# Kernel optimization log

Hardware: AMD Instinct MI355X
Metric: run time of the kernel (lower is better)

The kernel has to match this reference:

```python
import jax, jax.numpy as jnp
import numpy as np

B = 2048        # patients (segments)
K = 4           # images per patient
C = 1280        # backbone_out (tf_efficientnet_b0)
PAIRS = K * (K - 1) // 2  # torch.combinations -> 6
NCLS = 1
N_DROP = 5


def setup_inputs() -> dict:
    key = jax.random.key(0)
    ks = jax.random.split(key, 8)
    x = jax.random.normal(ks[0], (B * K, C), jnp.float32)  # detached backbone features
    ids2 = jnp.repeat(jnp.arange(B, dtype=jnp.int32), PAIRS)  # segment id per pair
    Wc = jax.random.normal(ks[1], (C, C, 2), jnp.float32) * 0.02  # Conv1d(C,C,k=2) weight
    bc = jnp.zeros((C,), jnp.float32)
    W0 = jax.random.normal(ks[2], (NCLS, C), jnp.float32) * 0.02
    b0 = jnp.zeros((NCLS,), jnp.float32)
    W1 = jax.random.normal(ks[3], (1, C), jnp.float32) * 0.02
    b1 = jnp.zeros((1,), jnp.float32)
    W2 = jax.random.normal(ks[4], (1, C), jnp.float32) * 0.02
    b2 = jnp.zeros((1,), jnp.float32)
    return dict(x=x, ids2=ids2, Wc=Wc, bc=bc, W0=W0, b0=b0, W1=W1, b1=b1, W2=W2, b2=b2)


def reference(x, ids2, Wc, bc, W0, b0, W1, b1, W2, b2):
    # --- pair combinations within each patient group of K images ---
    ii, jj = np.triu_indices(K, 1)               # static [PAIRS]
    xg = x.reshape(B, K, C)
    xa = xg[:, ii].reshape(B * PAIRS, C)         # first element of each pair
    xb = xg[:, jj].reshape(B * PAIRS, C)         # second element
    # Conv1d(C, C, kernel=2) over the length-2 pair sequence + ReLU
    xc = jax.nn.relu(xa @ Wc[:, :, 0].T + xb @ Wc[:, :, 1].T + bc)  # [P, C]

    # --- 5 fixed dropout masks (p=0.5, train-mode scaling) ---
    masks = jax.random.bernoulli(jax.random.key(42), 0.5,
                                 (N_DROP, xc.shape[0], C)).astype(xc.dtype) * 2.0
    xd = xc[None] * masks                        # [D, P, C]

    cnt = jax.ops.segment_sum(jnp.ones_like(ids2, dtype=xc.dtype),
                              ids2, num_segments=B)  # [B], == PAIRS

    def agg(W, b):
        # head -> scalar mean over classes -> segment-mean over pairs -> mean over dropouts
        z = (jnp.einsum('dpc,oc->dpo', xd, W) + b).mean(-1)          # [D, P]
        s = jax.vmap(lambda u: jax.ops.segment_sum(u, ids2, num_segments=B))(z)
        return (s / cnt).mean(0)                                      # [B]

    logits = agg(W0, b0)
    logits1 = agg(W1, b1)
    logits2 = agg(W2, b2)
    return jnp.stack([logits, logits1, logits2], axis=1)  # [B, 3]
```

## Files before the change

kernel.cpp:

```cpp
#include <hip/hip_runtime.h>


typedef __attribute__((ext_vector_type(8))) short short8;
typedef __attribute__((ext_vector_type(4))) float f32x4;

#define PLANE 15728640u
#define KS2   (0x1BD11BDAu ^ 42u)

__device__ __forceinline__ unsigned short f2bf(float f) {
  unsigned int u = __builtin_bit_cast(unsigned int, f);
  u = (u + 0x7FFFu + ((u >> 16) & 1u)) >> 16;
  return (unsigned short)u;
}

__global__ __launch_bounds__(256) void prep(
    const float* __restrict__ x, unsigned short* __restrict__ xb,
    const float* __restrict__ Wc, unsigned short* __restrict__ Wb,
    const float* __restrict__ b0, const float* __restrict__ b1,
    const float* __restrict__ b2, float* __restrict__ out) {
  const int bid = blockIdx.x;
  const int t = threadIdx.x;
  if (bid < 10240) {
    const int i = (bid * 256 + t) * 4;
    float4 v = *(const float4*)(x + i);
    ushort4 o;
    o.x = f2bf(v.x); o.y = f2bf(v.y); o.z = f2bf(v.z); o.w = f2bf(v.w);
    *(ushort4*)(xb + i) = o;
  } else if (bid < 23040) {
    const int idx = (bid - 10240) * 256 + t;
    const int n = idx / 2560;
    const int k = idx - n * 2560;
    const int side = (k >= 1280) ? 1 : 0;
    const int cin = k - side * 1280;
    Wb[idx] = f2bf(Wc[n * 2560 + cin * 2 + side]);
  } else {
    const int i = (bid - 23040) * 256 + t;
    if (i < 2048 * 3) {
      const int h = i % 3;
      out[i] = (h == 0) ? b0[0] : ((h == 1) ? b1[0] : b2[0]);
    }
  }
}

__device__ __forceinline__ unsigned int rotl(unsigned int x, int r) {
  return __builtin_amdgcn_alignbit(x, x, 32 - r);
}
__device__ __forceinline__ unsigned int tf_msb(unsigned int c) {
  unsigned int x0 = c;
  unsigned int x1 = rotl(c, 13) ^ c;
  x0 += x1; x1 = rotl(x1, 15) ^ x0;
  x0 += x1; x1 = rotl(x1, 26) ^ x0;
  x0 += x1; x1 = rotl(x1, 6)  ^ x0;
  unsigned int t;
  t = x1 + (KS2 + 1u); x0 = x0 + t + 42u; x1 = rotl(t, 17) ^ x0;
  x0 += x1; x1 = rotl(x1, 29) ^ x0;
  x0 += x1; x1 = rotl(x1, 16) ^ x0;
  x0 += x1; x1 = rotl(x1, 24) ^ x0;
  t = x1 + 2u; x0 = x0 + t + KS2; x1 = rotl(t, 13) ^ x0;
  x0 += x1; x1 = rotl(x1, 15) ^ x0;
  x0 += x1; x1 = rotl(x1, 26) ^ x0;
  x0 += x1; x1 = rotl(x1, 6)  ^ x0;
  t = x1 + 45u; x0 = x0 + t; x1 = rotl(t, 17) ^ x0;
  x0 += x1; x1 = rotl(x1, 29) ^ x0;
  x0 += x1; x1 = rotl(x1, 16) ^ x0;
  x0 += x1; x1 = rotl(x1, 24) ^ x0;
  t = x1 + (KS2 + 4u); x0 = x0 + t + 42u; x1 = rotl(t, 13) ^ x0;
  x0 += x1; x1 = rotl(x1, 15) ^ x0;
  x0 += x1; x1 = rotl(x1, 26) ^ x0;
  x0 += x1; x1 = rotl(x1, 6)  ^ x0;
  return ((x0 + KS2) ^ (x1 + 5u)) >> 31;
}

#define GL_LDS(g, l) __builtin_amdgcn_global_load_lds( \
    (const __attribute__((address_space(1))) unsigned int*)(g), \
    (__attribute__((address_space(3))) unsigned int*)(l), 16, 0, 0)

__global__ __launch_bounds__(256) void gemm_relu_dot(
    const unsigned short* __restrict__ Xb,
    const unsigned short* __restrict__ Wb,
    const float* __restrict__ bc,
    const float* __restrict__ W0, const float* __restrict__ W1,
    const float* __restrict__ W2, float* __restrict__ out)
{
  __shared__ unsigned short sA[128 * 32];
  __shared__ unsigned short sB[64 * 32];
  __shared__ unsigned int zLDS[4 * 256];
  __shared__ float rowsumA[128 * 3];
  __shared__ float rowsumB[128 * 3];

  const int t = threadIdx.x;
  const int id = blockIdx.x;
  const int mblk = id % 96;
  const int nblk = id / 96;
  const int p0 = mblk * 128, n0 = nblk * 64;
  const int lane = t & 63, w = t >> 6;
  const int wr = w >> 1, wc = w & 1;
  const int q = lane & 3;
  const int rl = lane >> 2;
  const int mrow = lane & 15;
  const int koff = (lane >> 4) * 8;
  const int mq = (lane >> 4) * 4;
  const int nn = lane & 15;

  int rA[2], rB[2];
#pragma unroll
  for (int i = 0; i < 2; i++) {
    const int row = w * 32 + i * 16 + rl;
    const int pg = p0 + row;
    const int bA = pg / 6, pr = pg - bA * 6;
    rA[i] = bA * 4 + ((0x211000 >> (4 * pr)) & 7);
    rB[i] = bA * 4 + ((0x332321 >> (4 * pr)) & 7);
  }
  const int rN = n0 + w * 16 + rl;

  unsigned short* const ldsA0 = sA + (w * 32 + 0) * 32;
  unsigned short* const ldsA1 = sA + (w * 32 + 16) * 32;
  unsigned short* const ldsB0 = sB + (w * 16) * 32;
  const unsigned short* const gA0s0 = Xb + rA[0] * 1280 + q * 8;
  const unsigned short* const gA1s0 = Xb + rA[1] * 1280 + q * 8;
  const unsigned short* const gA0s1 = Xb + rB[0] * 1280 + q * 8;
  const unsigned short* const gA1s1 = Xb + rB[1] * 1280 + q * 8;
  const unsigned short* const gB0 = Wb + rN * 2560 + q * 8;

  f32x4 acc[4][2];
#pragma unroll
  for (int i = 0; i < 4; i++)
#pragma unroll
    for (int j = 0; j < 2; j++) acc[i][j] = (f32x4){0.f, 0.f, 0.f, 0.f};

  const unsigned int tb =
      (unsigned int)((p0 + wr * 64 + mq) * 1280 + n0 + wc * 32 + nn) + 42u;

#define KSTEP(Ga0, Ga1, kb, kg)                                              \
  {                                                                          \
    __syncthreads();                                                         \
    GL_LDS(Ga0 + (kb), ldsA0);                                               \
    GL_LDS(Ga1 + (kb), ldsA1);                                               \
    GL_LDS(gB0 + (kg), ldsB0);                                               \
    __syncthreads();                                                         \
    short8 af[4], bfr[2];                                                    \
    _Pragma("unroll")                                                        \
    for (int i = 0; i < 4; i++)                                              \
      af[i] = *(const short8*)(sA + (wr * 64 + i * 16 + mrow) * 32 + koff);  \
    _Pragma("unroll")                                                        \
    for (int j = 0; j < 2; j++)                                              \
      bfr[j] = *(const short8*)(sB + (wc * 32 + j * 16 + mrow) * 32 + koff); \
    _Pragma("unroll")                                                        \
    for (int i = 0; i < 4; i++)                                              \
      _Pragma("unroll")                                                      \
      for (int j = 0; j < 2; j++)                                            \
        acc[i][j] = __builtin_amdgcn_mfma_f32_16x16x32_bf16(af[i], bfr[j],   \
                                                            acc[i][j], 0, 0, 0); \
  }

#define CELL_RNG(it)                                                         \
  {                                                                          \
    const int idx = (it);                                                    \
    const unsigned int b = tb +                                              \
        (unsigned int)((((idx >> 3) * 16 + (idx & 3)) * 1280) +              \
                       (((idx >> 2) & 1) * 16));                             \
    const unsigned int z5 = tf_msb(b) + tf_msb(b + PLANE) +                  \
                            tf_msb(b + 2u * PLANE) + tf_msb(b + 3u * PLANE) +\
                            tf_msb(b + 4u * PLANE);                          \
    zacc |= z5 << (4 * sub);                                                 \
  }

  for (int c8 = 0; c8 < 4; c8++) {
    unsigned int zacc = 0;
#pragma unroll
    for (int sub = 0; sub < 8; sub++) {
      const int it = c8 * 8 + sub;
      KSTEP(gA0s0, gA1s0, it * 32, it * 32);
      CELL_RNG(it);
    }
    zLDS[c8 * 256 + t] = zacc;
  }
  for (int it = 32; it < 40; it++) KSTEP(gA0s0, gA1s0, it * 32, it * 32);
  for (int it = 40; it < 80; it++) KSTEP(gA0s1, gA1s1, (it - 40) * 32, it * 32);
#undef KSTEP
#undef CELL_RNG

  unsigned int zq[4];
#pragma unroll
  for (int c = 0; c < 4; c++) zq[c] = zLDS[c * 256 + t];

  float w0v[2], w1v[2], w2v[2], bcv[2];
#pragma unroll
  for (int j = 0; j < 2; j++) {
    const int n = n0 + wc * 32 + j * 16 + nn;
    w0v[j] = W0[n]; w1v[j] = W1[n]; w2v[j] = W2[n]; bcv[j] = bc[n];
  }

  float* const dst = (wc == 0) ? rowsumA : rowsumB;
#pragma unroll
  for (int i = 0; i < 4; i++) {
#pragma unroll
    for (int rg = 0; rg < 4; rg++) {
      float s0 = 0.f, s1 = 0.f, s2 = 0.f;
#pragma unroll
      for (int j = 0; j < 2; j++) {
        const int idx = i * 8 + j * 4 + rg;
        const unsigned int z5 = (zq[idx >> 3] >> (4 * (idx & 7))) & 7u;
        float v = acc[i][j][rg] + bcv[j];
        v = v > 0.f ? v : 0.f;
        const float tx = v * (float)(5 - (int)z5);
        s0 += tx * w0v[j]; s1 += tx * w1v[j]; s2 += tx * w2v[j];
      }
#pragma unroll
      for (int off = 1; off < 16; off <<= 1) {
        s0 += __shfl_xor(s0, off);
        s1 += __shfl_xor(s1, off);
        s2 += __shfl_xor(s2, off);
      }
      if (nn == 0) {
        const int row = wr * 64 + i * 16 + mq + rg;
        dst[row * 3 + 0] = s0; dst[row * 3 + 1] = s1; dst[row * 3 + 2] = s2;
      }
    }
  }
  __syncthreads();

  if (t < 128) {
    const int pr = p0 + t;
    const int rem = pr % 6;
    if (t == 0 || rem == 0) {
      int nrows = 6 - rem;
      if (nrows > 128 - t) nrows = 128 - t;
      float a0 = 0.f, a1 = 0.f, a2 = 0.f;
      for (int k2 = 0; k2 < nrows; k2++) {
        a0 += rowsumA[(t + k2) * 3 + 0] + rowsumB[(t + k2) * 3 + 0];
        a1 += rowsumA[(t + k2) * 3 + 1] + rowsumB[(t + k2) * 3 + 1];
        a2 += rowsumA[(t + k2) * 3 + 2] + rowsumB[(t + k2) * 3 + 2];
      }
      const int pat = pr / 6;
      atomicAdd(&out[pat * 3 + 0], a0 * (1.0f / 15.0f));
      atomicAdd(&out[pat * 3 + 1], a1 * (1.0f / 15.0f));
      atomicAdd(&out[pat * 3 + 2], a2 * (1.0f / 15.0f));
    }
  }
}

extern "C" void kernel_launch(void* const* d_in, const int* in_sizes, int n_in,
                              void* d_out, int out_size, void* d_ws, size_t ws_size,
                              hipStream_t stream) {
  const float* x  = (const float*)d_in[0];
  const float* Wc = (const float*)d_in[2];
  const float* bc = (const float*)d_in[3];
  const float* W0 = (const float*)d_in[4];
  const float* b0 = (const float*)d_in[5];
  const float* W1 = (const float*)d_in[6];
  const float* b1 = (const float*)d_in[7];
  const float* W2 = (const float*)d_in[8];
  const float* b2 = (const float*)d_in[9];
  float* out = (float*)d_out;

  char* ws = (char*)d_ws;
  unsigned short* xb = (unsigned short*)ws;
  unsigned short* Wb = (unsigned short*)(ws + 20971520);

  prep<<<23064, 256, 0, stream>>>(x, xb, Wc, Wb, b0, b1, b2, out);
  gemm_relu_dot<<<1920, 256, 0, stream>>>(xb, Wb, bc, W0, W1, W2, out);
}
```

Baseline: 314.0 us.

## Load GEMM operands directly from global into registers, dropping LDS staging

The GEMM kernel now has each lane load its MFMA A and B fragments straight from global memory. This replaces the previous scheme of staging tiles into LDS with global_load_lds and two __syncthreads per k-step, and the dropout-mask bits are kept in registers instead of an LDS round trip. The goal is to remove barrier and LDS traffic overhead. In exchange, operand reuse across waves now depends on the L1/L2 caches, and each lane issues more, less coalesced 16-byte global loads.

```diff
diff --git a/kernel.cpp b/kernel.cpp
--- a/kernel.cpp
+++ b/kernel.cpp
@@ -71,10 +71,6 @@
   return ((x0 + KS2) ^ (x1 + 5u)) >> 31;
 }
 
-#define GL_LDS(g, l) __builtin_amdgcn_global_load_lds( \
-    (const __attribute__((address_space(1))) unsigned int*)(g), \
-    (__attribute__((address_space(3))) unsigned int*)(l), 16, 0, 0)
-
 __global__ __launch_bounds__(256) void gemm_relu_dot(
     const unsigned short* __restrict__ Xb,
     const unsigned short* __restrict__ Wb,
@@ -82,9 +78,6 @@
     const float* __restrict__ W0, const float* __restrict__ W1,
     const float* __restrict__ W2, float* __restrict__ out)
 {
-  __shared__ unsigned short sA[128 * 32];
-  __shared__ unsigned short sB[64 * 32];
-  __shared__ unsigned int zLDS[4 * 256];
   __shared__ float rowsumA[128 * 3];
   __shared__ float rowsumB[128 * 3];
 
@@ -95,32 +88,23 @@
   const int p0 = mblk * 128, n0 = nblk * 64;
   const int lane = t & 63, w = t >> 6;
   const int wr = w >> 1, wc = w & 1;
-  const int q = lane & 3;
-  const int rl = lane >> 2;
   const int mrow = lane & 15;
   const int koff = (lane >> 4) * 8;
   const int mq = (lane >> 4) * 4;
   const int nn = lane & 15;
 
-  int rA[2], rB[2];
-#pragma unroll
-  for (int i = 0; i < 2; i++) {
-    const int row = w * 32 + i * 16 + rl;
-    const int pg = p0 + row;
+  int rowA0[4], rowA1[4];
+#pragma unroll
+  for (int i = 0; i < 4; i++) {
+    const int pg = p0 + wr * 64 + i * 16 + mrow;
     const int bA = pg / 6, pr = pg - bA * 6;
-    rA[i] = bA * 4 + ((0x211000 >> (4 * pr)) & 7);
-    rB[i] = bA * 4 + ((0x332321 >> (4 * pr)) & 7);
-  }
-  const int rN = n0 + w * 16 + rl;
-
-  unsigned short* const ldsA0 = sA + (w * 32 + 0) * 32;
-  unsigned short* const ldsA1 = sA + (w * 32 + 16) * 32;
-  unsigned short* const ldsB0 = sB + (w * 16) * 32;
-  const unsigned short* const gA0s0 = Xb + rA[0] * 1280 + q * 8;
-  const unsigned short* const gA1s0 = Xb + rA[1] * 1280 + q * 8;
-  const unsigned short* const gA0s1 = Xb + rB[0] * 1280 + q * 8;
-  const unsigned short* const gA1s1 = Xb + rB[1] * 1280 + q * 8;
-  const unsigned short* const gB0 = Wb + rN * 2560 + q * 8;
+    rowA0[i] = bA * 4 + ((0x211000 >> (4 * pr)) & 7);
+    rowA1[i] = bA * 4 + ((0x332321 >> (4 * pr)) & 7);
+  }
+  const unsigned short* pB[2];
+#pragma unroll
+  for (int j = 0; j < 2; j++)
+    pB[j] = Wb + (n0 + wc * 32 + j * 16 + mrow) * 2560 + koff;
 
   f32x4 acc[4][2];
 #pragma unroll
@@ -130,21 +114,17 @@
 
   const unsigned int tb =
       (unsigned int)((p0 + wr * 64 + mq) * 1280 + n0 + wc * 32 + nn) + 42u;
-
-#define KSTEP(Ga0, Ga1, kb, kg)                                              \
+  unsigned int zq[4];
+
+#define LOAD_MFMA(pA, it)                                                    \
   {                                                                          \
-    __syncthreads();                                                         \
-    GL_LDS(Ga0 + (kb), ldsA0);                                               \
-    GL_LDS(Ga1 + (kb), ldsA1);                                               \
-    GL_LDS(gB0 + (kg), ldsB0);                                               \
-    __syncthreads();                                                         \
     short8 af[4], bfr[2];                                                    \
     _Pragma("unroll")                                                        \
     for (int i = 0; i < 4; i++)                                              \
-      af[i] = *(const short8*)(sA + (wr * 64 + i * 16 + mrow) * 32 + koff);  \
+      af[i] = *(const short8*)(pA[i] + (it) * 32);                           \
     _Pragma("unroll")                                                        \
     for (int j = 0; j < 2; j++)                                              \
-      bfr[j] = *(const short8*)(sB + (wc * 32 + j * 16 + mrow) * 32 + koff); \
+      bfr[j] = *(const short8*)(pB[j] + (it) * 32);                          \
     _Pragma("unroll")                                                        \
     for (int i = 0; i < 4; i++)                                              \
       _Pragma("unroll")                                                      \
@@ -165,24 +145,37 @@
     zacc |= z5 << (4 * sub);                                                 \
   }
 
-  for (int c8 = 0; c8 < 4; c8++) {
-    unsigned int zacc = 0;
-#pragma unroll
-    for (int sub = 0; sub < 8; sub++) {
-      const int it = c8 * 8 + sub;
-      KSTEP(gA0s0, gA1s0, it * 32, it * 32);
-      CELL_RNG(it);
-    }
-    zLDS[c8 * 256 + t] = zacc;
-  }
-  for (int it = 32; it < 40; it++) KSTEP(gA0s0, gA1s0, it * 32, it * 32);
-  for (int it = 40; it < 80; it++) KSTEP(gA0s1, gA1s1, (it - 40) * 32, it * 32);
-#undef KSTEP
+  {
+    const unsigned short* pA[4];
+#pragma unroll
+    for (int i = 0; i < 4; i++) pA[i] = Xb + rowA0[i] * 1280 + koff;
+    for (int c8 = 0; c8 < 4; c8++) {
+      unsigned int zacc = 0;
+#pragma unroll
+      for (int sub = 0; sub < 8; sub++) {
+        const int it = c8 * 8 + sub;
+        LOAD_MFMA(pA, it);
+        CELL_RNG(it);
+      }
+      zq[c8] = zacc;
+    }
+#pragma unroll
+    for (int it = 32; it < 40; it++) LOAD_MFMA(pA, it);
+  }
+  {
+    const unsigned short* pA[4];
+#pragma unroll
+    for (int i = 0; i < 4; i++) pA[i] = Xb + rowA1[i] * 1280 + koff - 40 * 32;
+    for (int c8 = 5; c8 < 10; c8++) {
+#pragma unroll
+      for (int sub = 0; sub < 8; sub++) {
+        const int it = c8 * 8 + sub;
+        LOAD_MFMA(pA, it);
+      }
+    }
+  }
+#undef LOAD_MFMA
 #undef CELL_RNG
-
-  unsigned int zq[4];
-#pragma unroll
-  for (int c = 0; c < 4; c++) zq[c] = zLDS[c * 256 + t];
 
   float w0v[2], w1v[2], w2v[2], bcv[2];
 #pragma unroll
```

New measurement: 459.4 us. 46.3% more time.

## Widen GEMM N tile to 128 and give each wave private LDS staging

Applied to the files above, without the earlier changes.

The GEMM block tile grows from 128x64 to 128x128, which halves the grid and doubles per-wave accumulators to 4x4 MFMA tiles. Each wave now loads its own A and B slices into a private LDS region, so the block-wide __syncthreads are replaced by s_waitcnt-based software prefetching of the next K step. The aim is more operand reuse per byte loaded and less barrier stall. In exchange, register and LDS pressure go up, A rows are loaded redundantly across waves, and fewer blocks are available to fill the CUs.

```diff
diff --git a/kernel.cpp b/kernel.cpp
--- a/kernel.cpp
+++ b/kernel.cpp
@@ -82,9 +82,8 @@
     const float* __restrict__ W0, const float* __restrict__ W1,
     const float* __restrict__ W2, float* __restrict__ out)
 {
-  __shared__ unsigned short sA[128 * 32];
-  __shared__ unsigned short sB[64 * 32];
-  __shared__ unsigned int zLDS[4 * 256];
+  __shared__ unsigned short sAB[4 * 4096];
+  __shared__ unsigned int zLDS[8 * 256];
   __shared__ float rowsumA[128 * 3];
   __shared__ float rowsumB[128 * 3];
 
@@ -92,102 +91,107 @@
   const int id = blockIdx.x;
   const int mblk = id % 96;
   const int nblk = id / 96;
-  const int p0 = mblk * 128, n0 = nblk * 64;
+  const int p0 = mblk * 128, n0 = nblk * 128;
   const int lane = t & 63, w = t >> 6;
   const int wr = w >> 1, wc = w & 1;
-  const int q = lane & 3;
-  const int rl = lane >> 2;
   const int mrow = lane & 15;
   const int koff = (lane >> 4) * 8;
   const int mq = (lane >> 4) * 4;
   const int nn = lane & 15;
 
-  int rA[2], rB[2];
-#pragma unroll
-  for (int i = 0; i < 2; i++) {
-    const int row = w * 32 + i * 16 + rl;
-    const int pg = p0 + row;
+  unsigned short* const wA = sAB + w * 4096;
+  unsigned short* const wB = wA + 2048;
+
+  const unsigned short* gA0[4];
+  const unsigned short* gA1[4];
+  const unsigned short* gB[4];
+#pragma unroll
+  for (int c = 0; c < 4; c++) {
+    const int pg = p0 + wr * 64 + c * 16 + (lane >> 2);
     const int bA = pg / 6, pr = pg - bA * 6;
-    rA[i] = bA * 4 + ((0x211000 >> (4 * pr)) & 7);
-    rB[i] = bA * 4 + ((0x332321 >> (4 * pr)) & 7);
-  }
-  const int rN = n0 + w * 16 + rl;
-
-  unsigned short* const ldsA0 = sA + (w * 32 + 0) * 32;
-  unsigned short* const ldsA1 = sA + (w * 32 + 16) * 32;
-  unsigned short* const ldsB0 = sB + (w * 16) * 32;
-  const unsigned short* const gA0s0 = Xb + rA[0] * 1280 + q * 8;
-  const unsigned short* const gA1s0 = Xb + rA[1] * 1280 + q * 8;
-  const unsigned short* const gA0s1 = Xb + rB[0] * 1280 + q * 8;
-  const unsigned short* const gA1s1 = Xb + rB[1] * 1280 + q * 8;
-  const unsigned short* const gB0 = Wb + rN * 2560 + q * 8;
-
-  f32x4 acc[4][2];
+    gA0[c] = Xb + (bA * 4 + ((0x211000 >> (4 * pr)) & 7)) * 1280 + (lane & 3) * 8;
+    gA1[c] = Xb + (bA * 4 + ((0x332321 >> (4 * pr)) & 7)) * 1280 + (lane & 3) * 8;
+    gB[c]  = Wb + (n0 + wc * 64 + c * 16 + (lane >> 2)) * 2560 + (lane & 3) * 8;
+  }
+
+  f32x4 acc[4][4];
 #pragma unroll
   for (int i = 0; i < 4; i++)
 #pragma unroll
-    for (int j = 0; j < 2; j++) acc[i][j] = (f32x4){0.f, 0.f, 0.f, 0.f};
+    for (int j = 0; j < 4; j++) acc[i][j] = (f32x4){0.f, 0.f, 0.f, 0.f};
 
   const unsigned int tb =
-      (unsigned int)((p0 + wr * 64 + mq) * 1280 + n0 + wc * 32 + nn) + 42u;
-
-#define KSTEP(Ga0, Ga1, kb, kg)                                              \
+      (unsigned int)((p0 + wr * 64 + mq) * 1280 + n0 + wc * 64 + nn) + 42u;
+
+#define STAGE(nxt)                                                           \
   {                                                                          \
-    __syncthreads();                                                         \
-    GL_LDS(Ga0 + (kb), ldsA0);                                               \
-    GL_LDS(Ga1 + (kb), ldsA1);                                               \
-    GL_LDS(gB0 + (kg), ldsB0);                                               \
-    __syncthreads();                                                         \
-    short8 af[4], bfr[2];                                                    \
+    const int _s1 = (nxt) >= 40;                                             \
+    const int _kA = ((nxt) - (_s1 ? 40 : 0)) * 32;                           \
+    const int _kB = (nxt) * 32;                                              \
+    _Pragma("unroll")                                                        \
+    for (int c = 0; c < 4; c++) {                                            \
+      GL_LDS((_s1 ? gA1[c] : gA0[c]) + _kA, wA + c * 512);                   \
+      GL_LDS(gB[c] + _kB, wB + c * 512);                                     \
+    }                                                                        \
+  }
+
+#define KSTEP(it)                                                            \
+  {                                                                          \
+    __builtin_amdgcn_s_waitcnt(0x0F70);       \
+    short8 af[4], bfr[4];                                                    \
     _Pragma("unroll")                                                        \
     for (int i = 0; i < 4; i++)                                              \
-      af[i] = *(const short8*)(sA + (wr * 64 + i * 16 + mrow) * 32 + koff);  \
-    _Pragma("unroll")                                                        \
-    for (int j = 0; j < 2; j++)                                              \
-      bfr[j] = *(const short8*)(sB + (wc * 32 + j * 16 + mrow) * 32 + koff); \
+      af[i] = *(const short8*)(wA + (i * 16 + mrow) * 32 + koff);            \
+    _Pragma("unroll")                                                        \
+    for (int j = 0; j < 4; j++)                                              \
+      bfr[j] = *(const short8*)(wB + (j * 16 + mrow) * 32 + koff);           \
     _Pragma("unroll")                                                        \
     for (int i = 0; i < 4; i++)                                              \
       _Pragma("unroll")                                                      \
-      for (int j = 0; j < 2; j++)                                            \
+      for (int j = 0; j < 4; j++)                                            \
         acc[i][j] = __builtin_amdgcn_mfma_f32_16x16x32_bf16(af[i], bfr[j],   \
                                                             acc[i][j], 0, 0, 0); \
+    __builtin_amdgcn_s_waitcnt(0xC07F);      \
+    if ((it) < 79) STAGE((it) + 1);                                          \
   }
 
 #define CELL_RNG(it)                                                         \
   {                                                                          \
     const int idx = (it);                                                    \
     const unsigned int b = tb +                                              \
-        (unsigned int)((((idx >> 3) * 16 + (idx & 3)) * 1280) +              \
-                       (((idx >> 2) & 1) * 16));                             \
+        (unsigned int)((((idx >> 4) * 16 + (idx & 3)) * 1280) +              \
+                       (((idx >> 2) & 3) * 16));                             \
     const unsigned int z5 = tf_msb(b) + tf_msb(b + PLANE) +                  \
                             tf_msb(b + 2u * PLANE) + tf_msb(b + 3u * PLANE) +\
                             tf_msb(b + 4u * PLANE);                          \
     zacc |= z5 << (4 * sub);                                                 \
   }
 
-  for (int c8 = 0; c8 < 4; c8++) {
+  STAGE(0);
+
+  for (int c8 = 0; c8 < 8; c8++) {
     unsigned int zacc = 0;
 #pragma unroll
     for (int sub = 0; sub < 8; sub++) {
       const int it = c8 * 8 + sub;
-      KSTEP(gA0s0, gA1s0, it * 32, it * 32);
+      KSTEP(it);
       CELL_RNG(it);
     }
     zLDS[c8 * 256 + t] = zacc;
   }
-  for (int it = 32; it < 40; it++) KSTEP(gA0s0, gA1s0, it * 32, it * 32);
-  for (int it = 40; it < 80; it++) KSTEP(gA0s1, gA1s1, (it - 40) * 32, it * 32);
+  for (int it = 64; it < 80; it++) KSTEP(it);
 #undef KSTEP
+#undef STAGE
 #undef CELL_RNG
 
-  unsigned int zq[4];
-#pragma unroll
-  for (int c = 0; c < 4; c++) zq[c] = zLDS[c * 256 + t];
-
-  float w0v[2], w1v[2], w2v[2], bcv[2];
-#pragma unroll
-  for (int j = 0; j < 2; j++) {
-    const int n = n0 + wc * 32 + j * 16 + nn;
+  unsigned int zq[8];
+#pragma unroll
+  for (int c = 0; c < 8; c++) zq[c] = zLDS[c * 256 + t];
+
+  float w0v[4], w1v[4], w2v[4], bcv[4];
+#pragma unroll
+  for (int j = 0; j < 4; j++) {
+    const int n = n0 + wc * 64 + j * 16 + nn;
     w0v[j] = W0[n]; w1v[j] = W1[n]; w2v[j] = W2[n]; bcv[j] = bc[n];
   }
 
@@ -198,8 +202,8 @@
     for (int rg = 0; rg < 4; rg++) {
       float s0 = 0.f, s1 = 0.f, s2 = 0.f;
 #pragma unroll
-      for (int j = 0; j < 2; j++) {
-        const int idx = i * 8 + j * 4 + rg;
+      for (int j = 0; j < 4; j++) {
+        const int idx = i * 16 + j * 4 + rg;
         const unsigned int z5 = (zq[idx >> 3] >> (4 * (idx & 7))) & 7u;
         float v = acc[i][j][rg] + bcv[j];
         v = v > 0.f ? v : 0.f;
@@ -259,5 +263,5 @@
   unsigned short* Wb = (unsigned short*)(ws + 20971520);
 
   prep<<<23064, 256, 0, stream>>>(x, xb, Wc, Wb, b0, b1, b2, out);
-  gemm_relu_dot<<<1920, 256, 0, stream>>>(xb, Wb, bc, W0, W1, W2, out);
-}
+  gemm_relu_dot<<<960, 256, 0, stream>>>(xb, Wb, bc, W0, W1, W2, out);
+}
```

Result: no change. 308.9 us (-1.7%).
